# Optimization experiments

Hardware: AMD Instinct MI355X
Metric: run time of the kernel (lower is better)

Reference implementation:

```python
import jax, jax.numpy as jnp
import numpy as np

H = 16
K = 64

def setup_inputs() -> dict:
    key = jax.random.key(0)
    k1, k2, k3 = jax.random.split(key, 3)
    b, m, d = 8, 1024, 1024
    x = jax.random.normal(k1, (b, m, d), dtype=jnp.float32)
    P_i = jax.random.normal(k2, (d, 3 * d), dtype=jnp.float32) * (1.0 / np.sqrt(d))
    P_o = jax.random.normal(k3, (d, d), dtype=jnp.float32) * (1.0 / np.sqrt(d))
    return {"x": x, "P_i": P_i, "P_o": P_o}

def reference(x, P_i, P_o):
    b, m, d = x.shape
    # fused QKV projection: [b, m, 3d] -> [b, m, h, 3k] -> [b, h, m, 3k]
    t = (x @ P_i).reshape(b, m, H, 3 * K).transpose(0, 2, 1, 3)
    Q, Kt, V = t[..., :K], t[..., K:2 * K], t[..., 2 * K:]
    logits = jnp.einsum('bhmk,bhnk->bhmn', Q, Kt) / jnp.sqrt(jnp.float32(K))
    # causal mask (tril): position m attends to n <= m
    causal = jnp.tril(jnp.ones((m, m), dtype=bool))
    logits = jnp.where(causal[None, None], logits, jnp.float32(-jnp.inf))
    w = jax.nn.softmax(logits, axis=-1)
    o = jnp.einsum('bhmn,bhnk->bhmk', w, V)  # [b, h, m, k]
    y = o.transpose(0, 2, 1, 3).reshape(b, m, H * K) @ P_o
    return y
```

## Files before the change

kernel.cpp:

```cpp
#include <hip/hip_runtime.h>

typedef unsigned short u16;
typedef __bf16 b16x8_t __attribute__((ext_vector_type(8)));
typedef unsigned short u16x8 __attribute__((ext_vector_type(8)));
typedef float f32x4 __attribute__((ext_vector_type(4)));

__device__ __forceinline__ u16 f2bf(float f) {
  union { float f; unsigned u; } x; x.f = f;
  unsigned r = x.u + 0x7fffu + ((x.u >> 16) & 1u);
  return (u16)(r >> 16);
}

__device__ __forceinline__ f32x4 mfma16(u16x8 a, u16x8 b, f32x4 c) {
  return __builtin_amdgcn_mfma_f32_16x16x32_bf16(
      __builtin_bit_cast(b16x8_t, a), __builtin_bit_cast(b16x8_t, b), c, 0, 0, 0);
}

__device__ __forceinline__ void gld_lds16(const void* g, void* l) {
  __builtin_amdgcn_global_load_lds(
      (const __attribute__((address_space(1))) void*)g,
      (__attribute__((address_space(3))) void*)l, 16, 0, 0);
}

__device__ __forceinline__ void store_out(float* p, float v) { *p = v; }
__device__ __forceinline__ void store_out(u16* p, float v) { *p = f2bf(v); }

__global__ void convert_bf16(const float* __restrict__ src, u16* __restrict__ dst, int n4) {
  int i = blockIdx.x * blockDim.x + threadIdx.x;
  if (i < n4) {
    float4 f = ((const float4*)src)[i];
    u16 a0 = f2bf(f.x), a1 = f2bf(f.y), a2 = f2bf(f.z), a3 = f2bf(f.w);
    unsigned lo = (unsigned)a0 | ((unsigned)a1 << 16);
    unsigned hi = (unsigned)a2 | ((unsigned)a3 << 16);
    ((uint2*)dst)[i] = make_uint2(lo, hi);
  }
}

__global__ void transpose_f32_bf16(const float* __restrict__ src, u16* __restrict__ dst,
                                   int R, int Cn) {
  __shared__ float t[32][33];
  int c0 = blockIdx.x * 32, r0 = blockIdx.y * 32;
  int tx = threadIdx.x, ty = threadIdx.y;
  for (int j = 0; j < 32; j += 8)
    t[ty + j][tx] = src[(size_t)(r0 + ty + j) * Cn + c0 + tx];
  __syncthreads();
  for (int j = 0; j < 32; j += 8)
    dst[(size_t)(c0 + ty + j) * R + r0 + tx] = f2bf(t[tx][ty + j]);
}

template <typename OutT, int BN, int EPI>
__global__ __launch_bounds__(256, 2) void gemm_v7(const u16* __restrict__ A,
                                                  const u16* __restrict__ Bt,
                                                  OutT* __restrict__ C,
                                                  u16* __restrict__ Vt,
                                                  int M, int N, int K) {
  constexpr int NB = BN / 64;
  constexpr int NJ = BN / 32;
  constexpr int NL = 2 + NB;
  __shared__ __align__(16) u16 sA[3][4096];
  __shared__ __align__(16) u16 sB[3][BN * 32];
  const int tid = threadIdx.x, lane = tid & 63, wid = tid >> 6;
  const int hi = lane >> 4, ln = lane & 15;
  const int wm = (wid >> 1) * 64, wn = (wid & 1) * (BN / 2);

  const int gdx = gridDim.x;
  const int nwg = gdx * gridDim.y;
  int wg = blockIdx.y * gdx + blockIdx.x;
  wg = (wg & 7) * (nwg >> 3) + (wg >> 3);
  const int m0 = (wg / gdx) * 128;
  const int n0 = (wg % gdx) * BN;

  const int sr = tid >> 2;
  const int scsw = ((tid & 3) ^ ((tid >> 3) & 3)) * 8;
  const u16* srcA = A + (size_t)(m0 + sr) * K + scsw;
  const u16* srcB = Bt + (size_t)(n0 + sr) * K + scsw;
  const size_t K64 = (size_t)64 * K;

  auto stage = [&](int buf, int t) {
    const int k0 = t * 32;
    gld_lds16(srcA + k0, &sA[buf][tid * 8]);
    gld_lds16(srcA + K64 + k0, &sA[buf][2048 + tid * 8]);
    gld_lds16(srcB + k0, &sB[buf][tid * 8]);
    gld_lds16(srcB + K64 + k0, &sB[buf][2048 + tid * 8]);
    if (NB > 2) gld_lds16(srcB + 2 * K64 + k0, &sB[buf][4096 + tid * 8]);
  };

  const int csw = (hi ^ ((ln >> 1) & 3)) * 8;
  int offA[4], offB[NJ];
#pragma unroll
  for (int i = 0; i < 4; ++i) offA[i] = (wm + i * 16 + ln) * 32 + csw;
#pragma unroll
  for (int j = 0; j < NJ; ++j) offB[j] = (wn + j * 16 + ln) * 32 + csw;

  f32x4 acc[4][NJ] = {};
  const int NT = K >> 5;

  stage(0, 0); stage(1, 1);
  if constexpr (NL == 5) asm volatile("s_waitcnt vmcnt(5)" ::: "memory");
  else                   asm volatile("s_waitcnt vmcnt(4)" ::: "memory");
  __builtin_amdgcn_s_barrier();

  int cb = 0, sb = 2;
  for (int kt = 0; kt < NT; ++kt) {
    u16x8 af[4], bf[NJ];
#pragma unroll
    for (int i = 0; i < 4; ++i) af[i] = *(const u16x8*)(&sA[cb][offA[i]]);
#pragma unroll
    for (int j = 0; j < NJ; ++j) bf[j] = *(const u16x8*)(&sB[cb][offB[j]]);
    if (kt + 2 < NT) {
      stage(sb, kt + 2);
      sb = (sb == 2) ? 0 : sb + 1;
      if constexpr (NL == 5) asm volatile("s_waitcnt vmcnt(5)" ::: "memory");
      else                   asm volatile("s_waitcnt vmcnt(4)" ::: "memory");
    } else {
      asm volatile("s_waitcnt vmcnt(0)" ::: "memory");
    }
    __builtin_amdgcn_s_barrier();
    asm volatile("s_waitcnt lgkmcnt(0)" ::: "memory");
    __builtin_amdgcn_sched_barrier(0);
    __builtin_amdgcn_s_setprio(1);
#pragma unroll
    for (int i = 0; i < 4; ++i)
#pragma unroll
      for (int j = 0; j < NJ; ++j)
        acc[i][j] = mfma16(af[i], bf[j], acc[i][j]);
    __builtin_amdgcn_s_setprio(0);
    __builtin_amdgcn_sched_barrier(0);
    __builtin_amdgcn_s_barrier();
    cb = (cb == 2) ? 0 : cb + 1;
  }

#pragma unroll
  for (int i = 0; i < 4; ++i) {
    int rr = m0 + wm + i * 16 + hi * 4;
#pragma unroll
    for (int j = 0; j < NJ; ++j) {
      int colw = wn + j * 16 + ln;
      if (EPI == 1 && colw >= 128) {
        int h = n0 / 192, kk = colw - 128;
        int b = rr >> 10, n = rr & 1023;
        ushort4 pk;
        pk.x = f2bf(acc[i][j][0]); pk.y = f2bf(acc[i][j][1]);
        pk.z = f2bf(acc[i][j][2]); pk.w = f2bf(acc[i][j][3]);
        *(ushort4*)(Vt + ((size_t)(b * 16 + h) * 64 + kk) * 1024 + n) = pk;
      } else {
        float sc = (EPI == 1 && colw < 64) ? 0.125f : 1.f;
        int col = n0 + colw;
#pragma unroll
        for (int r = 0; r < 4; ++r)
          store_out(&C[(size_t)(rr + r) * N + col], acc[i][j][r] * sc);
      }
    }
  }
}

__global__ __launch_bounds__(512, 4) void attn_fwd4(const u16* __restrict__ QKV,
                                                    const u16* __restrict__ Vt,
                                                    u16* __restrict__ O) {
  __shared__ __align__(16) u16 sK[2][4096];
  __shared__ __align__(16) u16 sVt[2][4096];
  __shared__ __align__(16) u16 sP[8][16 * 72];
  const int tid = threadIdx.x, lane = tid & 63, wid = tid >> 6;
  const int z = blockIdx.x, h = blockIdx.y, bb = blockIdx.z;
  const size_t rowbase = (size_t)bb * 1024;
  const size_t vbase = ((size_t)bb * 16 + h) * 64;
  const int colQ = h * 192, colK = colQ + 64;
  const int hi = lane >> 4, ln = lane & 15;
  const int slr = lane >> 3;
  const int sle = ((lane & 7) ^ slr) * 8;
  u16* sPw = sP[wid];
  const u16x8 onesf = {0x3F80, 0x3F80, 0x3F80, 0x3F80, 0x3F80, 0x3F80, 0x3F80, 0x3F80};

  auto stageKV = [&](int buf, int nt) {
    const int n0g = nt * 64;
    gld_lds16(QKV + (rowbase + n0g + 8 * wid + slr) * 3072 + colK + sle,
              &sK[buf][wid * 512]);
    gld_lds16(Vt + (vbase + 8 * wid + slr) * 1024 + n0g + sle,
              &sVt[buf][wid * 512]);
  };

  for (int half = 0; half < 2; ++half) {
    const int mt = half ? (7 - z) : z;
    const int qrow0 = mt * 128 + wid * 16;
    const int ntiles = 2 * mt + 2;

    u16x8 qf[2];
#pragma unroll
    for (int kb = 0; kb < 2; ++kb)
      qf[kb] = *(const u16x8*)(QKV + (rowbase + qrow0 + ln) * 3072 + colQ + kb * 32 + hi * 8);

    f32x4 o[4] = {};
    f32x4 lacc = {0.f, 0.f, 0.f, 0.f};
    float mrow[4];
#pragma unroll
    for (int r = 0; r < 4; ++r) mrow[r] = -1e30f;

    stageKV(0, 0);
    for (int nt = 0; nt < ntiles; ++nt) {
      __syncthreads();
      if (nt + 1 < ntiles) stageKV((nt + 1) & 1, nt + 1);
      const int buf = nt & 1;
      const int n0g = nt * 64;
      if (n0g <= qrow0 + 15) {
        f32x4 s[4] = {};
        __builtin_amdgcn_s_setprio(1);
#pragma unroll
        for (int kb = 0; kb < 2; ++kb)
#pragma unroll
          for (int j = 0; j < 4; ++j) {
            int row = j * 16 + ln;
            int cb = (kb * 64 + hi * 16) ^ ((row & 7) << 4);
            u16x8 kfr = *(const u16x8*)(&sK[buf][(row * 128 + cb) >> 1]);
            s[j] = mfma16(qf[kb], kfr, s[j]);
          }
        __builtin_amdgcn_s_setprio(0);
        if (n0g + 63 > qrow0) {
#pragma unroll
          for (int j = 0; j < 4; ++j) {
            int col = n0g + j * 16 + ln;
#pragma unroll
            for (int r = 0; r < 4; ++r)
              if (col > qrow0 + hi * 4 + r) s[j][r] = -3e38f;
          }
        }
        float tmv[4];
#pragma unroll
        for (int r = 0; r < 4; ++r) {
          float tm = fmaxf(fmaxf(s[0][r], s[1][r]), fmaxf(s[2][r], s[3][r]));
#pragma unroll
          for (int d = 1; d < 16; d <<= 1) tm = fmaxf(tm, __shfl_xor(tm, d, 64));
          tmv[r] = tm;
        }
        bool need = (tmv[0] > mrow[0] + 8.f) | (tmv[1] > mrow[1] + 8.f) |
                    (tmv[2] > mrow[2] + 8.f) | (tmv[3] > mrow[3] + 8.f);
        if (__any(need)) {
#pragma unroll
          for (int r = 0; r < 4; ++r) {
            float mnew = fmaxf(mrow[r], tmv[r]);
            float corr = __expf(mrow[r] - mnew);
            mrow[r] = mnew;
            lacc[r] *= corr;
#pragma unroll
            for (int dt = 0; dt < 4; ++dt) o[dt][r] *= corr;
          }
        }
#pragma unroll
        for (int j = 0; j < 4; ++j)
#pragma unroll
          for (int r = 0; r < 4; ++r)
            sPw[(hi * 4 + r) * 72 + j * 16 + ln] = f2bf(__expf(s[j][r] - mrow[r]));
        u16x8 pf[2];
#pragma unroll
        for (int kb2 = 0; kb2 < 2; ++kb2)
          pf[kb2] = *(const u16x8*)(&sPw[ln * 72 + kb2 * 32 + hi * 8]);
        __builtin_amdgcn_s_setprio(1);
        lacc = mfma16(pf[0], onesf, lacc);
        lacc = mfma16(pf[1], onesf, lacc);
#pragma unroll
        for (int dt = 0; dt < 4; ++dt)
#pragma unroll
          for (int kb2 = 0; kb2 < 2; ++kb2) {
            int row = dt * 16 + ln;
            int cb = (kb2 * 64 + hi * 16) ^ ((row & 7) << 4);
            u16x8 vfr = *(const u16x8*)(&sVt[buf][(row * 128 + cb) >> 1]);
            o[dt] = mfma16(pf[kb2], vfr, o[dt]);
          }
        __builtin_amdgcn_s_setprio(0);
      }
    }
#pragma unroll
    for (int r = 0; r < 4; ++r) {
      float inv = 1.f / lacc[r];
#pragma unroll
      for (int dt = 0; dt < 4; ++dt)
        O[(rowbase + qrow0 + hi * 4 + r) * 1024 + h * 64 + dt * 16 + ln] =
            f2bf(o[dt][r] * inv);
    }
  }
}

extern "C" void kernel_launch(void* const* d_in, const int* in_sizes, int n_in,
                              void* d_out, int out_size, void* d_ws, size_t ws_size,
                              hipStream_t stream) {
  const float* x = (const float*)d_in[0];
  const float* Pi = (const float*)d_in[1];
  const float* Po = (const float*)d_in[2];
  float* y = (float*)d_out;
  char* ws = (char*)d_ws;

  u16* qkv  = (u16*)(ws);
  u16* piT  = (u16*)(ws + 50331648);
  u16* poT  = (u16*)(ws + 56623104);
  u16* xbf  = (u16*)(ws + 58720256);
  u16* vt   = (u16*)(ws + 75497472);
  u16* obuf = (u16*)(ws + 58720256);

  convert_bf16<<<8192, 256, 0, stream>>>(x, xbf, 8388608 / 4);
  dim3 tb(32, 8);
  transpose_f32_bf16<<<dim3(96, 32), tb, 0, stream>>>(Pi, piT, 1024, 3072);
  transpose_f32_bf16<<<dim3(32, 32), tb, 0, stream>>>(Po, poT, 1024, 1024);

  gemm_v7<u16, 192, 1><<<dim3(16, 64), 256, 0, stream>>>(xbf, piT, qkv, vt,
                                                         8192, 3072, 1024);
  attn_fwd4<<<dim3(4, 16, 8), 512, 0, stream>>>(qkv, vt, obuf);
  gemm_v7<float, 128, 0><<<dim3(8, 64), 256, 0, stream>>>(obuf, poT, y, nullptr,
                                                          8192, 1024, 1024);
}
```

Baseline: 153.3 us.

## Add 8-wave 256x192 ping-pong QKV GEMM with interleaved LDS prefetch

Replaces the QKV projection GEMM with a new 512-thread kernel that computes 256x192 tiles. It double-buffers K-tiles of 64 in LDS, interleaves async global-to-LDS loads between MFMA clusters, and raises wave priority during the MFMA phases. The aim is to improve operand reuse and to overlap memory traffic with matrix math. The cost is larger LDS use, a register-heavy accumulator array, and tightly hand-scheduled barriers that could limit occupancy.

```diff
diff --git a/kernel.cpp b/kernel.cpp
--- a/kernel.cpp
+++ b/kernel.cpp
@@ -46,6 +46,144 @@
   __syncthreads();
   for (int j = 0; j < 32; j += 8)
     dst[(size_t)(c0 + ty + j) * R + r0 + tx] = f2bf(t[tx][ty + j]);
+}
+
+__global__ __launch_bounds__(512, 2) void gemm8p(const u16* __restrict__ A,
+                                                 const u16* __restrict__ Bt,
+                                                 u16* __restrict__ C,
+                                                 u16* __restrict__ Vt,
+                                                 int M, int N, int K) {
+  __shared__ __align__(16) u16 sA[2][16384];
+  __shared__ __align__(16) u16 sB[2][12288];
+  const int tid = threadIdx.x, lane = tid & 63, wid = tid >> 6;
+  const int hi = lane >> 4, ln = lane & 15;
+  const int wr = wid >> 2, wc = wid & 3;
+
+  const int gdx = gridDim.x;
+  const int nwg = gdx * gridDim.y;
+  int wg = blockIdx.y * gdx + blockIdx.x;
+  wg = (wg & 7) * (nwg >> 3) + (wg >> 3);
+  const int m0 = (wg / gdx) * 256;
+  const int n0 = (wg % gdx) * 192;
+
+  const int srow = tid >> 3;
+  const int sc = ((tid & 7) ^ (srow & 7)) * 8;
+  const u16* gA = A + (size_t)(m0 + srow) * K + sc;
+  const u16* gB = Bt + (size_t)(n0 + srow) * K + sc;
+  const size_t K64 = (size_t)64 * K;
+
+  auto stA = [&](int buf, int t, int q) {
+    gld_lds16(gA + (size_t)q * K64 + t * 64, &sA[buf][q * 4096 + tid * 8]);
+  };
+  auto stB = [&](int buf, int t, int q) {
+    gld_lds16(gB + (size_t)q * K64 + t * 64, &sB[buf][q * 4096 + tid * 8]);
+  };
+
+  int csw[2];
+  csw[0] = ((hi) ^ (ln & 7)) * 8;
+  csw[1] = ((4 + hi) ^ (ln & 7)) * 8;
+  const int aRow = (wr * 128 + ln) * 64;
+  const int bRow = (wc >> 1) * 6144 + ((wc & 1) * 48 + ln) * 64;
+
+  f32x4 acc[8][3] = {};
+  u16x8 af[4], bfk[3];
+
+  auto LDA = [&](int buf, int mq, int kk) {
+#pragma unroll
+    for (int i = 0; i < 4; ++i)
+      af[i] = *(const u16x8*)(&sA[buf][aRow + (mq * 64 + i * 16) * 64 + csw[kk]]);
+  };
+  auto LDB = [&](int buf, int kk) {
+#pragma unroll
+    for (int j = 0; j < 3; ++j)
+      bfk[j] = *(const u16x8*)(&sB[buf][bRow + (j * 16) * 64 + csw[kk]]);
+  };
+  auto PRE = [&] {
+    __builtin_amdgcn_s_barrier();
+    asm volatile("s_waitcnt lgkmcnt(0)" ::: "memory");
+    __builtin_amdgcn_sched_barrier(0);
+    __builtin_amdgcn_s_setprio(1);
+  };
+  auto POST = [&] {
+    __builtin_amdgcn_s_setprio(0);
+    __builtin_amdgcn_sched_barrier(0);
+    __builtin_amdgcn_s_barrier();
+  };
+  auto MMA12 = [&](int mq) {
+#pragma unroll
+    for (int i = 0; i < 4; ++i)
+#pragma unroll
+      for (int j = 0; j < 3; ++j)
+        acc[mq * 4 + i][j] = mfma16(af[i], bfk[j], acc[mq * 4 + i][j]);
+  };
+
+  const int NT = K >> 6;
+  stB(0, 0, 0); stB(0, 0, 1); stB(0, 0, 2);
+  stA(0, 0, 0); stA(0, 0, 1); stA(0, 0, 2); stA(0, 0, 3);
+  stB(1, 1, 0);
+  asm volatile("s_waitcnt vmcnt(1)" ::: "memory");
+  __builtin_amdgcn_s_barrier();
+
+  for (int it = 0; it < NT / 2; ++it) {
+    const int t1 = 2 * it + 1, t2 = 2 * it + 2, t3 = 2 * it + 3;
+    const bool s2 = t2 < NT, s3 = t3 < NT;
+    LDA(0, 0, 0); LDB(0, 0);
+    stB(1, t1, 1); stB(1, t1, 2); stA(1, t1, 0); stA(1, t1, 1);
+    PRE(); MMA12(0); POST();
+    LDA(0, 1, 0);
+    stA(1, t1, 2); stA(1, t1, 3);
+    PRE(); MMA12(1); POST();
+    LDA(0, 0, 1); LDB(0, 1);
+    PRE(); MMA12(0); POST();
+    LDA(0, 1, 1);
+    if (s2) stB(0, t2, 0);
+    PRE(); MMA12(1);
+    __builtin_amdgcn_s_setprio(0);
+    __builtin_amdgcn_sched_barrier(0);
+    if (s2) asm volatile("s_waitcnt vmcnt(1)" ::: "memory");
+    else    asm volatile("s_waitcnt vmcnt(0)" ::: "memory");
+    __builtin_amdgcn_s_barrier();
+    LDA(1, 0, 0); LDB(1, 0);
+    if (s2) { stB(0, t2, 1); stB(0, t2, 2); }
+    PRE(); MMA12(0); POST();
+    LDA(1, 1, 0);
+    if (s2) { stA(0, t2, 0); stA(0, t2, 1); }
+    PRE(); MMA12(1); POST();
+    LDA(1, 0, 1); LDB(1, 1);
+    if (s2) { stA(0, t2, 2); stA(0, t2, 3); }
+    PRE(); MMA12(0); POST();
+    LDA(1, 1, 1);
+    if (s3) stB(1, t3, 0);
+    PRE(); MMA12(1);
+    __builtin_amdgcn_s_setprio(0);
+    __builtin_amdgcn_sched_barrier(0);
+    if (s3) asm volatile("s_waitcnt vmcnt(1)" ::: "memory");
+    else    asm volatile("s_waitcnt vmcnt(0)" ::: "memory");
+    __builtin_amdgcn_s_barrier();
+  }
+
+#pragma unroll
+  for (int i = 0; i < 8; ++i) {
+    int rr = m0 + wr * 128 + i * 16 + hi * 4;
+#pragma unroll
+    for (int j = 0; j < 3; ++j) {
+      int colw = wc * 48 + j * 16 + ln;
+      if (colw >= 128) {
+        int h = n0 / 192, kk = colw - 128;
+        int b = rr >> 10, n = rr & 1023;
+        ushort4 pk;
+        pk.x = f2bf(acc[i][j][0]); pk.y = f2bf(acc[i][j][1]);
+        pk.z = f2bf(acc[i][j][2]); pk.w = f2bf(acc[i][j][3]);
+        *(ushort4*)(Vt + ((size_t)(b * 16 + h) * 64 + kk) * 1024 + n) = pk;
+      } else {
+        float sc2 = (colw < 64) ? 0.125f : 1.f;
+        int col = n0 + colw;
+#pragma unroll
+        for (int r = 0; r < 4; ++r)
+          store_out(&C[(size_t)(rr + r) * N + col], acc[i][j][r] * sc2);
+      }
+    }
+  }
 }
 
 template <typename OutT, int BN, int EPI>
@@ -300,8 +438,7 @@
   transpose_f32_bf16<<<dim3(96, 32), tb, 0, stream>>>(Pi, piT, 1024, 3072);
   transpose_f32_bf16<<<dim3(32, 32), tb, 0, stream>>>(Po, poT, 1024, 1024);
 
-  gemm_v7<u16, 192, 1><<<dim3(16, 64), 256, 0, stream>>>(xbf, piT, qkv, vt,
-                                                         8192, 3072, 1024);
+  gemm8p<<<dim3(16, 32), 512, 0, stream>>>(xbf, piT, qkv, vt, 8192, 3072, 1024);
   attn_fwd4<<<dim3(4, 16, 8), 512, 0, stream>>>(qkv, vt, obuf);
   gemm_v7<float, 128, 0><<<dim3(8, 64), 256, 0, stream>>>(obuf, poT, y, nullptr,
                                                           8192, 1024, 1024);
```

Result: no change. 153.1 us (-0.2%).

## Fuse fp32-to-bf16 conversion of x into the QKV projection GEMM

Applied to the files above, without the earlier changes.

Drops the separate convert_bf16 pass over x and adds a new QKV GEMM that loads fp32 A tiles into registers, converts them to bf16 and writes them into LDS itself. B still streams through direct global-to-LDS loads. The aim is to save a kernel launch plus a 32MB read and 16MB write of the bf16 copy of x. In exchange the GEMM reads twice as many bytes for A and spends VALU work and register pipelining with hand-placed waitcnts on conversion, which may slow the main loop.

```diff
diff --git a/kernel.cpp b/kernel.cpp
--- a/kernel.cpp
+++ b/kernel.cpp
@@ -24,17 +24,6 @@
 
 __device__ __forceinline__ void store_out(float* p, float v) { *p = v; }
 __device__ __forceinline__ void store_out(u16* p, float v) { *p = f2bf(v); }
-
-__global__ void convert_bf16(const float* __restrict__ src, u16* __restrict__ dst, int n4) {
-  int i = blockIdx.x * blockDim.x + threadIdx.x;
-  if (i < n4) {
-    float4 f = ((const float4*)src)[i];
-    u16 a0 = f2bf(f.x), a1 = f2bf(f.y), a2 = f2bf(f.z), a3 = f2bf(f.w);
-    unsigned lo = (unsigned)a0 | ((unsigned)a1 << 16);
-    unsigned hi = (unsigned)a2 | ((unsigned)a3 << 16);
-    ((uint2*)dst)[i] = make_uint2(lo, hi);
-  }
-}
 
 __global__ void transpose_f32_bf16(const float* __restrict__ src, u16* __restrict__ dst,
                                    int R, int Cn) {
@@ -46,6 +35,134 @@
   __syncthreads();
   for (int j = 0; j < 32; j += 8)
     dst[(size_t)(c0 + ty + j) * R + r0 + tx] = f2bf(t[tx][ty + j]);
+}
+
+__global__ __launch_bounds__(256, 2) void gemm_f32a(const float* __restrict__ A,
+                                                    const u16* __restrict__ Bt,
+                                                    u16* __restrict__ C,
+                                                    u16* __restrict__ Vt,
+                                                    int M, int N, int K) {
+  __shared__ __align__(16) u16 sA[3][4096];
+  __shared__ __align__(16) u16 sB[3][6144];
+  const int tid = threadIdx.x, lane = tid & 63, wid = tid >> 6;
+  const int hi = lane >> 4, ln = lane & 15;
+  const int wm = (wid >> 1) * 64, wn = (wid & 1) * 96;
+
+  const int gdx = gridDim.x;
+  const int nwg = gdx * gridDim.y;
+  int wg = blockIdx.y * gdx + blockIdx.x;
+  wg = (wg & 7) * (nwg >> 3) + (wg >> 3);
+  const int m0 = (wg / gdx) * 128;
+  const int n0 = (wg % gdx) * 192;
+
+  const int sr = tid >> 2;
+  const int sck = ((tid & 3) ^ ((tid >> 3) & 3)) * 8;
+  const float* srcA = A + (size_t)(m0 + sr) * K + sck;
+  const u16* srcB = Bt + (size_t)(n0 + sr) * K + sck;
+  const size_t K64 = (size_t)64 * K;
+
+  auto ldA4 = [&](int t, f32x4* d) {
+    const float* g = srcA + t * 32;
+    d[0] = *(const f32x4*)(g);
+    d[1] = *(const f32x4*)(g + 4);
+    d[2] = *(const f32x4*)(g + K64);
+    d[3] = *(const f32x4*)(g + K64 + 4);
+  };
+  auto wrA = [&](int buf, const f32x4* f) {
+    u16x8 v0, v1;
+#pragma unroll
+    for (int e = 0; e < 4; ++e) { v0[e] = f2bf(f[0][e]); v0[4 + e] = f2bf(f[1][e]); }
+#pragma unroll
+    for (int e = 0; e < 4; ++e) { v1[e] = f2bf(f[2][e]); v1[4 + e] = f2bf(f[3][e]); }
+    *(u16x8*)(&sA[buf][tid * 8]) = v0;
+    *(u16x8*)(&sA[buf][2048 + tid * 8]) = v1;
+  };
+  auto stB = [&](int buf, int t) {
+    const int k0 = t * 32;
+    gld_lds16(srcB + k0, &sB[buf][tid * 8]);
+    gld_lds16(srcB + K64 + k0, &sB[buf][2048 + tid * 8]);
+    gld_lds16(srcB + 2 * K64 + k0, &sB[buf][4096 + tid * 8]);
+  };
+
+  const int csw = (hi ^ ((ln >> 1) & 3)) * 8;
+  int offA[4], offB[6];
+#pragma unroll
+  for (int i = 0; i < 4; ++i) offA[i] = (wm + i * 16 + ln) * 32 + csw;
+#pragma unroll
+  for (int j = 0; j < 6; ++j) offB[j] = (wn + j * 16 + ln) * 32 + csw;
+
+  f32x4 acc[4][6] = {};
+  const int NT = K >> 5;
+
+  f32x4 afl[4];
+  {
+    f32x4 a0f[4];
+    ldA4(0, a0f);
+    ldA4(1, afl);
+    stB(0, 0);
+    stB(1, 1);
+    asm volatile("s_waitcnt vmcnt(10)" ::: "memory");
+    wrA(0, a0f);
+    asm volatile("s_waitcnt vmcnt(3)" ::: "memory");
+    asm volatile("s_waitcnt lgkmcnt(0)" ::: "memory");
+    __builtin_amdgcn_s_barrier();
+  }
+
+  int cb = 0, nb = 1, sb = 2;
+  for (int kt = 0; kt < NT; ++kt) {
+    u16x8 af[4], bf[6];
+#pragma unroll
+    for (int i = 0; i < 4; ++i) af[i] = *(const u16x8*)(&sA[cb][offA[i]]);
+#pragma unroll
+    for (int j = 0; j < 6; ++j) bf[j] = *(const u16x8*)(&sB[cb][offB[j]]);
+    if (kt + 1 < NT) {
+      asm volatile("s_waitcnt vmcnt(3)" ::: "memory");
+      wrA(nb, afl);
+    }
+    if (kt + 2 < NT) {
+      ldA4(kt + 2, afl);
+      stB(sb, kt + 2);
+      asm volatile("s_waitcnt vmcnt(7)" ::: "memory");
+    } else {
+      asm volatile("s_waitcnt vmcnt(0)" ::: "memory");
+    }
+    asm volatile("s_waitcnt lgkmcnt(0)" ::: "memory");
+    __builtin_amdgcn_sched_barrier(0);
+    __builtin_amdgcn_s_barrier();
+    __builtin_amdgcn_sched_barrier(0);
+    __builtin_amdgcn_s_setprio(1);
+#pragma unroll
+    for (int i = 0; i < 4; ++i)
+#pragma unroll
+      for (int j = 0; j < 6; ++j)
+        acc[i][j] = mfma16(af[i], bf[j], acc[i][j]);
+    __builtin_amdgcn_s_setprio(0);
+    __builtin_amdgcn_sched_barrier(0);
+    int t = cb; cb = nb; nb = sb; sb = t;
+  }
+
+#pragma unroll
+  for (int i = 0; i < 4; ++i) {
+    int rr = m0 + wm + i * 16 + hi * 4;
+#pragma unroll
+    for (int j = 0; j < 6; ++j) {
+      int colw = wn + j * 16 + ln;
+      if (colw >= 128) {
+        int h = n0 / 192, kk = colw - 128;
+        int b = rr >> 10, n = rr & 1023;
+        ushort4 pk;
+        pk.x = f2bf(acc[i][j][0]); pk.y = f2bf(acc[i][j][1]);
+        pk.z = f2bf(acc[i][j][2]); pk.w = f2bf(acc[i][j][3]);
+        *(ushort4*)(Vt + ((size_t)(b * 16 + h) * 64 + kk) * 1024 + n) = pk;
+      } else {
+        float sc = (colw < 64) ? 0.125f : 1.f;
+        int col = n0 + colw;
+#pragma unroll
+        for (int r = 0; r < 4; ++r)
+          store_out(&C[(size_t)(rr + r) * N + col], acc[i][j][r] * sc);
+      }
+    }
+  }
 }
 
 template <typename OutT, int BN, int EPI>
@@ -136,20 +253,11 @@
 #pragma unroll
     for (int j = 0; j < NJ; ++j) {
       int colw = wn + j * 16 + ln;
-      if (EPI == 1 && colw >= 128) {
-        int h = n0 / 192, kk = colw - 128;
-        int b = rr >> 10, n = rr & 1023;
-        ushort4 pk;
-        pk.x = f2bf(acc[i][j][0]); pk.y = f2bf(acc[i][j][1]);
-        pk.z = f2bf(acc[i][j][2]); pk.w = f2bf(acc[i][j][3]);
-        *(ushort4*)(Vt + ((size_t)(b * 16 + h) * 64 + kk) * 1024 + n) = pk;
-      } else {
-        float sc = (EPI == 1 && colw < 64) ? 0.125f : 1.f;
-        int col = n0 + colw;
-#pragma unroll
-        for (int r = 0; r < 4; ++r)
-          store_out(&C[(size_t)(rr + r) * N + col], acc[i][j][r] * sc);
-      }
+      float sc = (EPI == 1 && colw < 64) ? 0.125f : 1.f;
+      int col = n0 + colw;
+#pragma unroll
+      for (int r = 0; r < 4; ++r)
+        store_out(&C[(size_t)(rr + r) * N + col], acc[i][j][r] * sc);
     }
   }
 }
@@ -291,17 +399,14 @@
   u16* qkv  = (u16*)(ws);
   u16* piT  = (u16*)(ws + 50331648);
   u16* poT  = (u16*)(ws + 56623104);
-  u16* xbf  = (u16*)(ws + 58720256);
+  u16* obuf = (u16*)(ws + 58720256);
   u16* vt   = (u16*)(ws + 75497472);
-  u16* obuf = (u16*)(ws + 58720256);
-
-  convert_bf16<<<8192, 256, 0, stream>>>(x, xbf, 8388608 / 4);
+
   dim3 tb(32, 8);
   transpose_f32_bf16<<<dim3(96, 32), tb, 0, stream>>>(Pi, piT, 1024, 3072);
   transpose_f32_bf16<<<dim3(32, 32), tb, 0, stream>>>(Po, poT, 1024, 1024);
 
-  gemm_v7<u16, 192, 1><<<dim3(16, 64), 256, 0, stream>>>(xbf, piT, qkv, vt,
-                                                         8192, 3072, 1024);
+  gemm_f32a<<<dim3(16, 64), 256, 0, stream>>>(x, piT, qkv, vt, 8192, 3072, 1024);
   attn_fwd4<<<dim3(4, 16, 8), 512, 0, stream>>>(qkv, vt, obuf);
   gemm_v7<float, 128, 0><<<dim3(8, 64), 256, 0, stream>>>(obuf, poT, y, nullptr,
                                                           8192, 1024, 1024);
```

Result: no change. 153.1 us (-0.1%).
